# Kernel tuning notes

Measured on AMD Instinct MI355X. Metric: run time of the kernel, lower is better.

## Reference

```python
import jax, jax.numpy as jnp
import numpy as np

N, E, D = 50000, 800000, 128
H, C = 8, 16  # heads, hidden_per_head; H*C == D
NEG_SLOPE = 0.15


def setup_inputs() -> dict:
    key = jax.random.key(0)
    ks = jax.random.split(key, 8)
    x = jax.random.normal(ks[0], (N, D), dtype=jnp.float32)
    edge_index = jax.random.randint(ks[1], (2, E), 0, N, dtype=jnp.int32)
    s = 1.0 / np.sqrt(D)
    return {
        "x": x,
        "edge_index": edge_index,
        "ln_g": jnp.ones((D,), jnp.float32),
        "ln_b": jnp.zeros((D,), jnp.float32),
        "W_l": jax.random.normal(ks[2], (D, H * C), jnp.float32) * s,
        "b_l": jnp.zeros((H * C,), jnp.float32),
        "W_r": jax.random.normal(ks[3], (D, H * C), jnp.float32) * s,
        "b_r": jnp.zeros((H * C,), jnp.float32),
        "att": jax.random.normal(ks[4], (H, C), jnp.float32) * (1.0 / np.sqrt(C)),
        "bias": jnp.zeros((H * C,), jnp.float32),
    }


def _layernorm(x, g, b, eps=1e-5):
    mu = jnp.mean(x, axis=-1, keepdims=True)
    var = jnp.mean(jnp.square(x - mu), axis=-1, keepdims=True)
    return (x - mu) * jax.lax.rsqrt(var + eps) * g + b


def reference(x, edge_index, ln_g, ln_b, W_l, b_l, W_r, b_r, att, bias):
    src, dst = edge_index[0], edge_index[1]
    h = _layernorm(x, ln_g, ln_b)                      # [N, D]
    xl = (h @ W_l + b_l).reshape(N, H, C)              # source-side transform
    xr = (h @ W_r + b_r).reshape(N, H, C)              # target-side transform
    # GATv2 edge attention: leaky_relu(x_j + x_i) . att
    e = xl[src] + xr[dst]                              # [E, H, C]
    e_act = jnp.where(e > 0, e, NEG_SLOPE * e)
    alpha = jnp.einsum('ehc,hc->eh', e_act, att)       # [E, H]
    # segment softmax over edges grouped by destination node
    m = jax.ops.segment_max(alpha, dst, num_segments=N)   # [N, H]
    ex = jnp.exp(alpha - m[dst])                           # [E, H]
    denom = jax.ops.segment_sum(ex, dst, num_segments=N)  # [N, H]
    a = ex / (denom[dst] + 1e-16)                          # [E, H]
    # weighted message aggregation (scatter-add)
    msg = xl[src] * a[:, :, None]                          # [E, H, C]
    out = jax.ops.segment_sum(msg, dst, num_segments=N)   # [N, H, C]
    out = out.reshape(N, H * C) + bias
    h2 = jax.nn.relu(out)                                  # act='relu', dropout off (eval)
    return x + h2                                          # proj is Identity (in_dim == out_dim)
```

## Files before the change

### kernel.cpp

```cpp
#include <hip/hip_runtime.h>

typedef unsigned int uint32;
typedef __attribute__((ext_vector_type(4))) float f32x4;
typedef __attribute__((ext_vector_type(2))) float f32x2;
typedef __attribute__((ext_vector_type(8))) short bf16x8;
typedef __attribute__((ext_vector_type(4))) uint32 u32x4;

#define NEG_SLOPE 0.15f
#define GPB 2
#define SBUF_MAX 4096
#define CSR_MAX  6144

__device__ __forceinline__ float2 bf2_to_f2(uint32 u) {
  union { uint32 i; float f; } a, b;
  a.i = u << 16;
  b.i = u & 0xffff0000u;
  return make_float2(a.f, b.f);
}

__device__ __forceinline__ f32x2 unpk(uint32 u) {
  union { uint32 i; float f; } lo, hi;
  lo.i = u << 16; hi.i = u & 0xffff0000u;
  f32x2 r; r.x = lo.f; r.y = hi.f; return r;
}

__device__ __forceinline__ float bf_to_f(unsigned short s) {
  union { uint32 i; float f; } u;
  u.i = ((uint32)s) << 16;
  return u.f;
}

__device__ __forceinline__ unsigned short f32_to_bf16(float f) {
  union { float f; uint32 i; } u; u.f = f;
  uint32 r = u.i + 0x7fffu + ((u.i >> 16) & 1u);
  return (unsigned short)(r >> 16);
}

__device__ __forceinline__ uint32 pack_bf2(float x, float y) {
  return (uint32)f32_to_bf16(x) | ((uint32)f32_to_bf16(y) << 16);
}

__device__ __forceinline__ float2 loadpair(const void* p, size_t i, int isbf) {
  if (isbf) return bf2_to_f2(((const uint32*)p)[i]);
  return ((const float2*)p)[i];
}

__device__ __forceinline__ float2 loadpair_nt(const void* p, size_t i, int isbf) {
  if (isbf) {
    uint32 u = __builtin_nontemporal_load((const uint32*)p + i);
    return bf2_to_f2(u);
  }
  f32x2 v = __builtin_nontemporal_load((const f32x2*)p + i);
  return make_float2(v.x, v.y);
}

__device__ __forceinline__ float loadelem(const void* p, size_t i, int isbf) {
  if (isbf) return bf_to_f(((const unsigned short*)p)[i]);
  return ((const float*)p)[i];
}

__device__ __forceinline__ int get_isbf(const void* ln_g) {
  return ((const uint32*)ln_g)[0] != 0x3F800000u ? 1 : 0;
}

__device__ __forceinline__ float dpp_swap1(float x) {
  union { float f; int i; } u, r;
  u.f = x;
  r.i = __builtin_amdgcn_mov_dpp(u.i, 0xB1, 0xF, 0xF, false);
  return r.f;
}

__device__ __forceinline__ f32x2 pk_add(f32x2 a, f32x2 b) {
  f32x2 d;
  asm("v_pk_add_f32 %0, %1, %2" : "=v"(d) : "v"(a), "v"(b));
  return d;
}
__device__ __forceinline__ f32x2 pk_mul(f32x2 a, f32x2 b) {
  f32x2 d;
  asm("v_pk_mul_f32 %0, %1, %2" : "=v"(d) : "v"(a), "v"(b));
  return d;
}
__device__ __forceinline__ f32x2 pk_fma(f32x2 a, f32x2 b, f32x2 c) {
  f32x2 d;
  asm("v_pk_fma_f32 %0, %1, %2, %3" : "=v"(d) : "v"(a), "v"(b), "v"(c));
  return d;
}
__device__ __forceinline__ float exp2_raw(float x) {
  float r;
  asm("v_exp_f32 %0, %1" : "=v"(r) : "v"(x));
  return r;
}

__global__ __launch_bounds__(256) void prep_hist_k(
    const void* __restrict__ Wl, const void* __restrict__ Wr,
    const void* __restrict__ bl, const void* __restrict__ br,
    const void* __restrict__ att, const void* __restrict__ obias,
    const void* __restrict__ ln_g, const void* __restrict__ ln_b,
    unsigned short* __restrict__ Wt, float* __restrict__ c1,
    float* __restrict__ c2b, float* __restrict__ att_c,
    float* __restrict__ obias_c,
    const int* __restrict__ ei, int* __restrict__ cntg,
    int E, int Eb, int R)
{
  int b = blockIdx.x;
  if (b < 128) {
    int isbf = get_isbf(ln_g);
    int id = b * 256 + threadIdx.x;
    int n = id >> 7, k = id & 127;
    float g = loadelem(ln_g, k, isbf);
    float v = (n < 128) ? loadelem(Wl, (size_t)k * 128 + n, isbf)
                        : loadelem(Wr, (size_t)k * 128 + (n - 128), isbf);
    Wt[(size_t)n * 128 + k] = f32_to_bf16(g * v);
    if (id < 128) {
      att_c[id]   = loadelem(att, id, isbf) * 1.44269504088896f;
      obias_c[id] = loadelem(obias, id, isbf);
    }
  } else if (b < 192) {
    int isbf = get_isbf(ln_g);
    int w = threadIdx.x >> 6, lane = threadIdx.x & 63;
    int n = (b - 128) * 4 + w;
    const void* W = (n < 128) ? Wl : Wr;
    int nn = n & 127;
    float s1 = 0.f, s2 = 0.f;
    #pragma unroll
    for (int t = 0; t < 2; ++t) {
      int kk = t * 64 + lane;
      float wv = loadelem(W, (size_t)kk * 128 + nn, isbf);
      s1 += loadelem(ln_g, kk, isbf) * wv;
      s2 += loadelem(ln_b, kk, isbf) * wv;
    }
    #pragma unroll
    for (int off = 1; off < 64; off <<= 1) {
      s1 += __shfl_xor(s1, off, 64);
      s2 += __shfl_xor(s2, off, 64);
    }
    if (lane == 0) {
      c1[n] = s1;
      c2b[n] = s2 + ((n < 128) ? loadelem(bl, nn, isbf) : loadelem(br, nn, isbf));
    }
  } else {
    __shared__ int hist[256];
    int hb = b - 192, tid = threadIdx.x;
    hist[tid] = 0;
    __syncthreads();
    int startE = hb * Eb, endE = min(E, startE + Eb);
    const int* dp = ei + E;
    int nfull = (endE > startE) ? ((endE - startE) >> 2) : 0;
    for (int g = tid; g < nfull; g += 256) {
      int4 d = *(const int4*)(dp + startE + g * 4);
      atomicAdd(&hist[((uint32)d.x) >> 8], 1);
      atomicAdd(&hist[((uint32)d.y) >> 8], 1);
      atomicAdd(&hist[((uint32)d.z) >> 8], 1);
      atomicAdd(&hist[((uint32)d.w) >> 8], 1);
    }
    int rem0 = startE + nfull * 4;
    if (rem0 + tid < endE) atomicAdd(&hist[((uint32)dp[rem0 + tid]) >> 8], 1);
    __syncthreads();
    if (tid < R) cntg[tid * 256 + hb] = hist[tid];
  }
}

__global__ __launch_bounds__(1024) void scanA_k(const int* __restrict__ in,
    int* __restrict__ outl, int* __restrict__ psum, int n)
{
  __shared__ int wsum[16];
  int tid = threadIdx.x, lane = tid & 63, w = tid >> 6;
  int i = blockIdx.x * 1024 + tid;
  int v = (i < n) ? in[i] : 0;
  int xs = v;
  #pragma unroll
  for (int off = 1; off < 64; off <<= 1) {
    int y = __shfl_up(xs, off, 64);
    if (lane >= off) xs += y;
  }
  if (lane == 63) wsum[w] = xs;
  __syncthreads();
  if (w == 0) {
    int sv = (lane < 16) ? wsum[lane] : 0;
    int ss = sv;
    #pragma unroll
    for (int off = 1; off < 16; off <<= 1) {
      int y = __shfl_up(ss, off, 64);
      if (lane >= off) ss += y;
    }
    if (lane < 16) wsum[lane] = ss - sv;
    if (lane == 15) psum[blockIdx.x] = ss;
  }
  __syncthreads();
  if (i < n) outl[i] = wsum[w] + xs - v;
}

__device__ __forceinline__ void load_group(bf16x8* slot, const void* x,
                                           int isbf, int rl, int quad) {
  if (isbf) {
    const unsigned short* xp = (const unsigned short*)x + (size_t)rl * 128 + quad * 8;
    #pragma unroll
    for (int kc = 0; kc < 4; ++kc) slot[kc] = *(const bf16x8*)(xp + kc * 32);
  } else {
    const float* xp = (const float*)x + (size_t)rl * 128 + quad * 8;
    #pragma unroll
    for (int kc = 0; kc < 4; ++kc) {
      float4 a0 = *(const float4*)(xp + kc * 32);
      float4 a1 = *(const float4*)(xp + kc * 32 + 4);
      union { bf16x8 v; uint32 u[4]; } av;
      av.u[0] = pack_bf2(a0.x, a0.y);
      av.u[1] = pack_bf2(a0.z, a0.w);
      av.u[2] = pack_bf2(a1.x, a1.y);
      av.u[3] = pack_bf2(a1.z, a1.w);
      slot[kc] = av.v;
    }
  }
}

__global__ __launch_bounds__(256) void bin_gemm_k(
    const int* __restrict__ ei, const int* __restrict__ cntg,
    const int* __restrict__ cbase,
    const int* __restrict__ psum, uint32* __restrict__ binned,
    int E, int Eb, int R, int nbScan,
    const void* __restrict__ x, const void* __restrict__ ln_g,
    const unsigned short* __restrict__ Wt,
    const float* __restrict__ c1, const float* __restrict__ c2b,
    unsigned short* __restrict__ xl, unsigned short* __restrict__ xr,
    int nrows)
{
  if (blockIdx.x < 256) {
    __shared__ int spsum[64];
    __shared__ int wsum2[4];
    __shared__ int lofs[256];
    __shared__ int gbase[256];
    __shared__ int cur[256];
    __shared__ uint32 sbuf[SBUF_MAX];
    int b = blockIdx.x, tid = threadIdx.x;
    int lane = tid & 63, w = tid >> 6;

    if (tid < 64) {
      int v = (tid < nbScan) ? psum[tid] : 0;
      int xs = v;
      #pragma unroll
      for (int off = 1; off < 64; off <<= 1) {
        int y = __shfl_up(xs, off, 64);
        if (tid >= off) xs += y;
      }
      spsum[tid] = xs - v;
    }
    int v2 = (tid < R) ? cntg[tid * 256 + b] : 0;
    int xs2 = v2;
    #pragma unroll
    for (int off = 1; off < 64; off <<= 1) {
      int y = __shfl_up(xs2, off, 64);
      if (lane >= off) xs2 += y;
    }
    if (lane == 63) wsum2[w] = xs2;
    __syncthreads();

    int woff2 = 0;
    #pragma unroll
    for (int i = 0; i < 4; ++i) if (i < w) woff2 += wsum2[i];
    int lo = woff2 + xs2 - v2;
    lofs[tid] = lo;
    int startE = b * Eb, endE = min(E, startE + Eb);
    if (tid < R) {
      int idx = tid * 256 + b;
      gbase[tid] = cbase[idx] + spsum[idx >> 10];
    }

    if (Eb <= SBUF_MAX) {
      cur[tid] = lo;
      __syncthreads();
      for (int e = startE + tid; e < endE; e += 256) {
        uint32 src = (uint32)ei[e], dst = (uint32)ei[E + e];
        uint32 r = dst >> 8;
        int pos = atomicAdd(&cur[r], 1);
        sbuf[pos] = src | ((dst & 255u) << 16) | (r << 24);
      }
      __syncthreads();
      int nloc = endE - startE;
      for (int i = tid; i < nloc; i += 256) {
        uint32 e2 = sbuf[i];
        uint32 r = e2 >> 24;
        binned[gbase[r] + (i - lofs[r])] = e2 & 0x00FFFFFFu;
      }
    } else {
      cur[tid] = (tid < R) ? gbase[tid] : 0;
      __syncthreads();
      for (int e = startE + tid; e < endE; e += 256) {
        uint32 src = (uint32)ei[e], dst = (uint32)ei[E + e];
        int pos = atomicAdd(&cur[dst >> 8], 1);
        binned[pos] = src | ((dst & 255u) << 16);
      }
    }
    return;
  }

  __shared__ unsigned short ot[4][16][72];
  int bid  = blockIdx.x - 256;
  int isbf = get_isbf(ln_g);
  int lane = threadIdx.x & 63;
  int w    = threadIdx.x >> 6;
  int m16  = lane & 15;
  int quad = lane >> 4;
  int base = bid * (GPB * 16);

  bf16x8 araw[GPB][4];
  #pragma unroll
  for (int g2 = 0; g2 < GPB; ++g2) {
    int r = base + g2 * 16 + m16;
    if (r >= nrows) r = nrows - 1;
    load_group(araw[g2], x, isbf, r, quad);
  }

  bf16x8 bfrag[4][4];
  #pragma unroll
  for (int nt = 0; nt < 4; ++nt)
    #pragma unroll
    for (int kc = 0; kc < 4; ++kc)
      bfrag[nt][kc] = *(const bf16x8*)(
          Wt + (size_t)(w * 64 + nt * 16 + m16) * 128 + kc * 32 + quad * 8);

  float c1v[4], c2v[4];
  #pragma unroll
  for (int nt = 0; nt < 4; ++nt) {
    int col = w * 64 + nt * 16 + m16;
    c1v[nt] = c1[col];
    c2v[nt] = c2b[col];
  }

  unsigned short* dst = (w < 2) ? xl : xr;
  int cb = (w & 1) * 64;

  #pragma unroll
  for (int g2 = 0; g2 < GPB; ++g2) {
    bf16x8* A = araw[g2];

    float s = 0.f, s2 = 0.f;
    #pragma unroll
    for (int kc = 0; kc < 4; ++kc) {
      union { bf16x8 v; uint32 u[4]; } uu; uu.v = A[kc];
      #pragma unroll
      for (int j = 0; j < 4; ++j) {
        float2 t = bf2_to_f2(uu.u[j]);
        s += t.x + t.y;
        s2 += t.x * t.x + t.y * t.y;
      }
    }
    s  += __shfl_xor(s, 16, 64);  s2 += __shfl_xor(s2, 16, 64);
    s  += __shfl_xor(s, 32, 64);  s2 += __shfl_xor(s2, 32, 64);
    float mu  = s * (1.0f / 128.0f);
    float var = fmaxf(s2 * (1.0f / 128.0f) - mu * mu, 0.0f);
    float rs  = rsqrtf(var + 1e-5f);
    float rm  = rs * mu;

    f32x4 acc[4];
    #pragma unroll
    for (int nt = 0; nt < 4; ++nt) acc[nt] = (f32x4){0.f, 0.f, 0.f, 0.f};
    #pragma unroll
    for (int kc = 0; kc < 4; ++kc)
      #pragma unroll
      for (int nt = 0; nt < 4; ++nt)
        acc[nt] = __builtin_amdgcn_mfma_f32_16x16x32_bf16(A[kc], bfrag[nt][kc], acc[nt], 0, 0, 0);

    float rs_j[4], rm_j[4];
    #pragma unroll
    for (int j = 0; j < 4; ++j) {
      rs_j[j] = __shfl(rs, quad * 4 + j, 64);
      rm_j[j] = __shfl(rm, quad * 4 + j, 64);
    }

    #pragma unroll
    for (int nt = 0; nt < 4; ++nt) {
      #pragma unroll
      for (int j = 0; j < 4; ++j) {
        ot[w][quad * 4 + j][nt * 16 + m16] =
            f32_to_bf16(rs_j[j] * acc[nt][j] - rm_j[j] * c1v[nt] + c2v[nt]);
      }
    }
    #pragma unroll
    for (int h = 0; h < 2; ++h) {
      int row16 = h * 8 + (lane >> 3);
      int cp    = lane & 7;
      int r = base + g2 * 16 + row16;
      bf16x8 v = *(const bf16x8*)&ot[w][row16][cp * 8];
      if (r < nrows)
        *(bf16x8*)(dst + (size_t)r * 128 + cb + cp * 8) = v;
    }
  }
}

__global__ __launch_bounds__(1024) void rangesort_k(
    const uint32* __restrict__ binned, const int* __restrict__ cbase,
    const int* __restrict__ psum,
    int* __restrict__ starts, unsigned short* __restrict__ csr16,
    int E, int N, int R, int nbScan)
{
  __shared__ int hist[256];
  __shared__ int wsum[4];
  __shared__ int cur[256];
  __shared__ int spsum[64];
  __shared__ unsigned short csr_l[CSR_MAX];
  int r = blockIdx.x;
  int tid = threadIdx.x, lane = tid & 63, w = tid >> 6;

  if (tid < 64) {
    int pv = (tid < nbScan) ? psum[tid] : 0;
    int pxs = pv;
    #pragma unroll
    for (int off = 1; off < 64; off <<= 1) {
      int y = __shfl_up(pxs, off, 64);
      if (tid >= off) pxs += y;
    }
    spsum[tid] = pxs - pv;
  }
  if (tid < 256) hist[tid] = 0;
  __syncthreads();

  int i0 = r * 256;
  int segStart = cbase[i0] + spsum[i0 >> 10];
  int segEnd;
  if (r + 1 < R) {
    int i1 = (r + 1) * 256;
    segEnd = cbase[i1] + spsum[i1 >> 10];
  } else {
    segEnd = E;
  }
  int segLen = segEnd - segStart;
  bool lds_ok = (segLen <= CSR_MAX);
  if (r == 0) {
    if (tid == 0) starts[N] = E;
    if (tid < 32) csr16[E + tid] = 0;
  }

  for (int i = segStart + tid; i < segEnd; i += 1024)
    atomicAdd(&hist[(binned[i] >> 16) & 255u], 1);
  __syncthreads();

  int v = 0, xs = 0;
  if (tid < 256) {
    v = hist[tid];
    xs = v;
    #pragma unroll
    for (int off = 1; off < 64; off <<= 1) {
      int y = __shfl_up(xs, off, 64);
      if (lane >= off) xs += y;
    }
    if (lane == 63) wsum[w] = xs;
  }
  __syncthreads();
  if (tid < 256) {
    int woff = 0;
    #pragma unroll
    for (int i = 0; i < 4; ++i) if (i < w) woff += wsum[i];
    int st_local = woff + xs - v;
    int node = (r << 8) + tid;
    if (node < N) starts[node] = segStart + st_local;
    cur[tid] = lds_ok ? st_local : segStart + st_local;
  }
  __syncthreads();

  if (lds_ok) {
    for (int i = segStart + tid; i < segEnd; i += 1024) {
      uint32 pk = binned[i];
      int d = (pk >> 16) & 255u;
      int pos = atomicAdd(&cur[d], 1);
      csr_l[pos] = (unsigned short)(pk & 0xffffu);
    }
    __syncthreads();
    for (int i = tid; i < segLen; i += 1024)
      csr16[segStart + i] = csr_l[i];
  } else {
    for (int i = segStart + tid; i < segEnd; i += 1024) {
      uint32 pk = binned[i];
      int d = (pk >> 16) & 255u;
      int pos = atomicAdd(&cur[d], 1);
      csr16[pos] = (unsigned short)(pk & 0xffffu);
    }
  }
}

__global__ __launch_bounds__(256) void agg_k(
    const uint32* __restrict__ xl32,
    const uint32* __restrict__ xr32,
    const int* __restrict__ starts, const unsigned short* __restrict__ csr16,
    const void* __restrict__ x, const void* __restrict__ ln_g,
    const float* __restrict__ att_c, const float* __restrict__ obias_c,
    void* __restrict__ out, int n)
{
  int node = blockIdx.x * 4 + (threadIdx.x >> 6);
  if (node >= n) return;
  int isbf = get_isbf(ln_g);
  int lane = threadIdx.x & 63;
  int q    = lane >> 4;
  int sub  = lane & 15;

  u32x4 xru = __builtin_nontemporal_load(
      (const u32x4*)(xr32 + (size_t)node * 64 + sub * 4));
  f32x2 xr0 = unpk(xru.x), xr1 = unpk(xru.y), xr2 = unpk(xru.z), xr3 = unpk(xru.w);
  const f32x2* atp = (const f32x2*)(att_c + sub * 8);
  f32x2 t0 = atp[0], t1 = atp[1], t2 = atp[2], t3 = atp[3];
  f32x2 ns; ns.x = NEG_SLOPE; ns.y = NEG_SLOPE;

  float lsum = 0.f;
  f32x2 ac[4];
  #pragma unroll
  for (int i = 0; i < 4; ++i) { ac[i].x = 0.f; ac[i].y = 0.f; }

  int p0 = __builtin_amdgcn_readfirstlane(starts[node]);
  int p1 = __builtin_amdgcn_readfirstlane(starts[node + 1]);

#define AGG_BODY(XU, OK) do { \
    f32x2 a0 = unpk((XU).x), a1 = unpk((XU).y), a2 = unpk((XU).z), a3 = unpk((XU).w); \
    f32x2 e0 = pk_add(a0, xr0), e1 = pk_add(a1, xr1); \
    f32x2 e2 = pk_add(a2, xr2), e3 = pk_add(a3, xr3); \
    f32x2 m0 = pk_mul(e0, ns), m1 = pk_mul(e1, ns); \
    f32x2 m2 = pk_mul(e2, ns), m3 = pk_mul(e3, ns); \
    e0.x = fmaxf(e0.x, m0.x); e0.y = fmaxf(e0.y, m0.y); \
    e1.x = fmaxf(e1.x, m1.x); e1.y = fmaxf(e1.y, m1.y); \
    e2.x = fmaxf(e2.x, m2.x); e2.y = fmaxf(e2.y, m2.y); \
    e3.x = fmaxf(e3.x, m3.x); e3.y = fmaxf(e3.y, m3.y); \
    f32x2 dt = pk_mul(e0, t0); \
    dt = pk_fma(e1, t1, dt); \
    dt = pk_fma(e2, t2, dt); \
    dt = pk_fma(e3, t3, dt); \
    float dot = dt.x + dt.y; \
    dot += dpp_swap1(dot); \
    float pw = (OK) ? exp2_raw(dot) : 0.f; \
    lsum += pw; \
    f32x2 pw2; pw2.x = pw; pw2.y = pw; \
    ac[0] = pk_fma(pw2, a0, ac[0]); \
    ac[1] = pk_fma(pw2, a1, ac[1]); \
    ac[2] = pk_fma(pw2, a2, ac[2]); \
    ac[3] = pk_fma(pw2, a3, ac[3]); \
  } while (0)

  if (p0 < p1) {
    uint32 so = (uint32)(sub * 4);
    const unsigned short* csp = csr16 + p0 + q;
    uint32 j0 = csp[0];
    uint32 j1 = csp[4];
    uint32 j2 = csp[8];
    uint32 j3 = csp[12];
    uint4 xu0 = *(const uint4*)(xl32 + (size_t)(j0 * 64u + so));
    uint4 xu1 = *(const uint4*)(xl32 + (size_t)(j1 * 64u + so));
    int pq   = p0 + q;
    int p1m4 = p1 - 4;
    for (int p = p0; p < p1; p += 8) {
      uint4 xA = xu0;
      xu0 = *(const uint4*)(xl32 + (size_t)(j2 * 64u + so));
      j2  = csp[16];
      AGG_BODY(xA, pq < p1);
      uint4 xB = xu1;
      xu1 = *(const uint4*)(xl32 + (size_t)(j3 * 64u + so));
      j3  = csp[20];
      AGG_BODY(xB, pq < p1m4);
      csp += 8;
      pq  += 8;
    }
  }
#undef AGG_BODY

  lsum += __shfl_xor(lsum, 16, 64);
  lsum += __shfl_xor(lsum, 32, 64);
  #pragma unroll
  for (int i = 0; i < 4; ++i) {
    ac[i].x += __shfl_xor(ac[i].x, 16, 64);
    ac[i].x += __shfl_xor(ac[i].x, 32, 64);
    ac[i].y += __shfl_xor(ac[i].y, 16, 64);
    ac[i].y += __shfl_xor(ac[i].y, 32, 64);
  }

  if (q == 0) {
    float inv = 1.0f / (lsum + 1e-16f);
    float4 b0 = *(const float4*)(obias_c + sub * 8);
    float4 b1 = *(const float4*)(obias_c + sub * 8 + 4);
    float2 rx[4];
    #pragma unroll
    for (int i = 0; i < 4; ++i)
      rx[i] = loadpair_nt(x, (size_t)node * 64 + sub * 4 + i, isbf);
    float o0 = rx[0].x + fmaxf(ac[0].x * inv + b0.x, 0.f);
    float o1 = rx[0].y + fmaxf(ac[0].y * inv + b0.y, 0.f);
    float o2 = rx[1].x + fmaxf(ac[1].x * inv + b0.z, 0.f);
    float o3 = rx[1].y + fmaxf(ac[1].y * inv + b0.w, 0.f);
    float o4 = rx[2].x + fmaxf(ac[2].x * inv + b1.x, 0.f);
    float o5 = rx[2].y + fmaxf(ac[2].y * inv + b1.y, 0.f);
    float o6 = rx[3].x + fmaxf(ac[3].x * inv + b1.z, 0.f);
    float o7 = rx[3].y + fmaxf(ac[3].y * inv + b1.w, 0.f);
    if (isbf) {
      u32x4 ov;
      ov.x = pack_bf2(o0, o1); ov.y = pack_bf2(o2, o3);
      ov.z = pack_bf2(o4, o5); ov.w = pack_bf2(o6, o7);
      __builtin_nontemporal_store(ov, (u32x4*)((uint32*)out + (size_t)node * 64 + sub * 4));
    } else {
      f32x4 f0; f0.x = o0; f0.y = o1; f0.z = o2; f0.w = o3;
      f32x4 f1; f1.x = o4; f1.y = o5; f1.z = o6; f1.w = o7;
      __builtin_nontemporal_store(f0, (f32x4*)((float*)out + (size_t)node * 128 + sub * 8));
      __builtin_nontemporal_store(f1, (f32x4*)((float*)out + (size_t)node * 128 + sub * 8 + 4));
    }
  }
}

static inline char* align16(char* p) {
  return (char*)(((uintptr_t)p + 15) & ~(uintptr_t)15);
}

extern "C" void kernel_launch(void* const* d_in, const int* in_sizes, int n_in,
                              void* d_out, int out_size, void* d_ws, size_t ws_size,
                              hipStream_t stream) {
  const void* x    = d_in[0];
  const int*  ei   = (const int*)d_in[1];
  const void* ln_g = d_in[2];
  const void* ln_b = d_in[3];
  const void* Wl   = d_in[4];
  const void* bl   = d_in[5];
  const void* Wr   = d_in[6];
  const void* br   = d_in[7];
  const void* att  = d_in[8];
  const void* bias = d_in[9];

  int N = in_sizes[0] / 128;
  int E = in_sizes[1] / 2;
  int R = (N + 255) >> 8;
  int L = R * 256;
  int Eb = (((E + 255) / 256) + 3) & ~3;

  char* ws = (char*)d_ws;
  unsigned short* xl = (unsigned short*)ws; ws = align16(ws + (size_t)N * 128 * 2);
  unsigned short* xr = (unsigned short*)ws; ws = align16(ws + (size_t)N * 128 * 2);
  unsigned short* Wt = (unsigned short*)ws; ws = align16(ws + 256 * 128 * 2);
  float* c1      = (float*)ws;              ws = align16(ws + 256 * 4);
  float* c2b     = (float*)ws;              ws = align16(ws + 256 * 4);
  float* att_c   = (float*)ws;              ws = align16(ws + 128 * 4);
  float* obias_c = (float*)ws;              ws = align16(ws + 128 * 4);
  int* cntg      = (int*)ws;                ws = align16(ws + (size_t)L * 4);
  int* cbase     = (int*)ws;                ws = align16(ws + (size_t)L * 4);
  int* psum      = (int*)ws;                ws = align16(ws + 64 * 4);
  int* starts    = (int*)ws;                ws = align16(ws + (size_t)(N + 1) * 4);
  uint32* binned = (uint32*)ws;             ws = align16(ws + (size_t)E * 4);
  unsigned short* csr16 = (unsigned short*)ws; ws = align16(ws + (size_t)(E + 32) * 2);

  int nbScan = (L + 1023) / 1024;
  int nGemmB = (N + GPB * 16 - 1) / (GPB * 16);

  hipLaunchKernelGGL(prep_hist_k, dim3(448), dim3(256), 0, stream,
                     Wl, Wr, bl, br, att, bias, ln_g, ln_b,
                     Wt, c1, c2b, att_c, obias_c,
                     ei, cntg, E, Eb, R);
  hipLaunchKernelGGL(scanA_k, dim3(nbScan), dim3(1024), 0, stream, cntg, cbase, psum, L);
  hipLaunchKernelGGL(bin_gemm_k, dim3(256 + nGemmB), dim3(256), 0, stream,
                     ei, cntg, cbase, psum, binned, E, Eb, R, nbScan,
                     x, ln_g, Wt, c1, c2b, xl, xr, N);
  hipLaunchKernelGGL(rangesort_k, dim3(R), dim3(1024), 0, stream,
                     binned, cbase, psum, starts, csr16, E, N, R, nbScan);
  hipLaunchKernelGGL(agg_k, dim3((N + 3) / 4), dim3(256), 0, stream,
                     (const uint32*)xl, (const uint32*)xr, starts, csr16,
                     x, ln_g, att_c, obias_c, d_out, N);
}
```

Before: 170.5 us.

## Replace global scan kernel with per-range atomic totals and atomic slot reservation

Removes the scanA_k launch. The histogram blocks now atomically accumulate per-range totals, and each binning block scans those totals locally and reserves its slice within each range with an atomicAdd on a global cursor. The rangesort kernel derives its segment bounds from the same totals. This saves one kernel launch and the scan pass, but adds a memset and makes the order of edges within each range nondeterministic. That is harmless as long as rangesort fully re-sorts within each range.

After: 174.7 us. 1.02x slower.

```diff
diff --git a/kernel.cpp b/kernel.cpp
--- a/kernel.cpp
+++ b/kernel.cpp
@@ -100,6 +100,7 @@
     float* __restrict__ c2b, float* __restrict__ att_c,
     float* __restrict__ obias_c,
     const int* __restrict__ ei, int* __restrict__ cntg,
+    int* __restrict__ rtot,
     int E, int Eb, int R)
 {
   int b = blockIdx.x;
@@ -156,38 +157,12 @@
     int rem0 = startE + nfull * 4;
     if (rem0 + tid < endE) atomicAdd(&hist[((uint32)dp[rem0 + tid]) >> 8], 1);
     __syncthreads();
-    if (tid < R) cntg[tid * 256 + hb] = hist[tid];
-  }
-}
-
-__global__ __launch_bounds__(1024) void scanA_k(const int* __restrict__ in,
-    int* __restrict__ outl, int* __restrict__ psum, int n)
-{
-  __shared__ int wsum[16];
-  int tid = threadIdx.x, lane = tid & 63, w = tid >> 6;
-  int i = blockIdx.x * 1024 + tid;
-  int v = (i < n) ? in[i] : 0;
-  int xs = v;
-  #pragma unroll
-  for (int off = 1; off < 64; off <<= 1) {
-    int y = __shfl_up(xs, off, 64);
-    if (lane >= off) xs += y;
-  }
-  if (lane == 63) wsum[w] = xs;
-  __syncthreads();
-  if (w == 0) {
-    int sv = (lane < 16) ? wsum[lane] : 0;
-    int ss = sv;
-    #pragma unroll
-    for (int off = 1; off < 16; off <<= 1) {
-      int y = __shfl_up(ss, off, 64);
-      if (lane >= off) ss += y;
-    }
-    if (lane < 16) wsum[lane] = ss - sv;
-    if (lane == 15) psum[blockIdx.x] = ss;
-  }
-  __syncthreads();
-  if (i < n) outl[i] = wsum[w] + xs - v;
+    if (tid < R) {
+      int h = hist[tid];
+      cntg[tid * 256 + hb] = h;
+      if (h) atomicAdd(&rtot[tid], h);
+    }
+  }
 }
 
 __device__ __forceinline__ void load_group(bf16x8* slot, const void* x,
@@ -214,9 +189,9 @@
 
 __global__ __launch_bounds__(256) void bin_gemm_k(
     const int* __restrict__ ei, const int* __restrict__ cntg,
-    const int* __restrict__ cbase,
-    const int* __restrict__ psum, uint32* __restrict__ binned,
-    int E, int Eb, int R, int nbScan,
+    const int* __restrict__ rtot, int* __restrict__ gcur,
+    uint32* __restrict__ binned,
+    int E, int Eb, int R,
     const void* __restrict__ x, const void* __restrict__ ln_g,
     const unsigned short* __restrict__ Wt,
     const float* __restrict__ c1, const float* __restrict__ c2b,
@@ -224,8 +199,9 @@
     int nrows)
 {
   if (blockIdx.x < 256) {
-    __shared__ int spsum[64];
-    __shared__ int wsum2[4];
+    __shared__ int wsumA[4];
+    __shared__ int wsumB[4];
+    __shared__ int rb[256];
     __shared__ int lofs[256];
     __shared__ int gbase[256];
     __shared__ int cur[256];
@@ -233,16 +209,14 @@
     int b = blockIdx.x, tid = threadIdx.x;
     int lane = tid & 63, w = tid >> 6;
 
-    if (tid < 64) {
-      int v = (tid < nbScan) ? psum[tid] : 0;
-      int xs = v;
-      #pragma unroll
-      for (int off = 1; off < 64; off <<= 1) {
-        int y = __shfl_up(xs, off, 64);
-        if (tid >= off) xs += y;
-      }
-      spsum[tid] = xs - v;
-    }
+    int rt = (tid < R) ? rtot[tid] : 0;
+    int xs1 = rt;
+    #pragma unroll
+    for (int off = 1; off < 64; off <<= 1) {
+      int y = __shfl_up(xs1, off, 64);
+      if (lane >= off) xs1 += y;
+    }
+    if (lane == 63) wsumA[w] = xs1;
     int v2 = (tid < R) ? cntg[tid * 256 + b] : 0;
     int xs2 = v2;
     #pragma unroll
@@ -250,19 +224,21 @@
       int y = __shfl_up(xs2, off, 64);
       if (lane >= off) xs2 += y;
     }
-    if (lane == 63) wsum2[w] = xs2;
+    if (lane == 63) wsumB[w] = xs2;
     __syncthreads();
 
-    int woff2 = 0;
-    #pragma unroll
-    for (int i = 0; i < 4; ++i) if (i < w) woff2 += wsum2[i];
-    int lo = woff2 + xs2 - v2;
+    int woffA = 0, woffB = 0;
+    #pragma unroll
+    for (int i = 0; i < 4; ++i) {
+      if (i < w) { woffA += wsumA[i]; woffB += wsumB[i]; }
+    }
+    rb[tid] = woffA + xs1 - rt;
+    int lo = woffB + xs2 - v2;
     lofs[tid] = lo;
+    int res = 0;
+    if (tid < R && v2 > 0) res = atomicAdd(&gcur[tid], v2);
+    gbase[tid] = rb[tid] + res;
     int startE = b * Eb, endE = min(E, startE + Eb);
-    if (tid < R) {
-      int idx = tid * 256 + b;
-      gbase[tid] = cbase[idx] + spsum[idx >> 10];
-    }
 
     if (Eb <= SBUF_MAX) {
       cur[tid] = lo;
@@ -281,7 +257,7 @@
         binned[gbase[r] + (i - lofs[r])] = e2 & 0x00FFFFFFu;
       }
     } else {
-      cur[tid] = (tid < R) ? gbase[tid] : 0;
+      cur[tid] = gbase[tid];
       __syncthreads();
       for (int e = startE + tid; e < endE; e += 256) {
         uint32 src = (uint32)ei[e], dst = (uint32)ei[E + e];
@@ -387,41 +363,41 @@
 }
 
 __global__ __launch_bounds__(1024) void rangesort_k(
-    const uint32* __restrict__ binned, const int* __restrict__ cbase,
-    const int* __restrict__ psum,
+    const uint32* __restrict__ binned, const int* __restrict__ rtot,
     int* __restrict__ starts, unsigned short* __restrict__ csr16,
-    int E, int N, int R, int nbScan)
+    int E, int N, int R)
 {
   __shared__ int hist[256];
   __shared__ int wsum[4];
+  __shared__ int wsumR[4];
   __shared__ int cur[256];
-  __shared__ int spsum[64];
+  __shared__ int segb[2];
   __shared__ unsigned short csr_l[CSR_MAX];
   int r = blockIdx.x;
   int tid = threadIdx.x, lane = tid & 63, w = tid >> 6;
 
-  if (tid < 64) {
-    int pv = (tid < nbScan) ? psum[tid] : 0;
-    int pxs = pv;
+  int rt = 0, xsr = 0;
+  if (tid < 256) {
+    rt = (tid < R) ? rtot[tid] : 0;
+    xsr = rt;
     #pragma unroll
     for (int off = 1; off < 64; off <<= 1) {
-      int y = __shfl_up(pxs, off, 64);
-      if (tid >= off) pxs += y;
-    }
-    spsum[tid] = pxs - pv;
-  }
-  if (tid < 256) hist[tid] = 0;
+      int y = __shfl_up(xsr, off, 64);
+      if (lane >= off) xsr += y;
+    }
+    if (lane == 63) wsumR[w] = xsr;
+    hist[tid] = 0;
+  }
   __syncthreads();
-
-  int i0 = r * 256;
-  int segStart = cbase[i0] + spsum[i0 >> 10];
-  int segEnd;
-  if (r + 1 < R) {
-    int i1 = (r + 1) * 256;
-    segEnd = cbase[i1] + spsum[i1 >> 10];
-  } else {
-    segEnd = E;
-  }
+  if (tid < 256) {
+    int woff = 0;
+    #pragma unroll
+    for (int i = 0; i < 4; ++i) if (i < w) woff += wsumR[i];
+    int ex = woff + xsr - rt;
+    if (tid == r) { segb[0] = ex; segb[1] = ex + rt; }
+  }
+  __syncthreads();
+  int segStart = segb[0], segEnd = segb[1];
   int segLen = segEnd - segStart;
   bool lds_ok = (segLen <= CSR_MAX);
   if (r == 0) {
@@ -630,25 +606,24 @@
   float* att_c   = (float*)ws;              ws = align16(ws + 128 * 4);
   float* obias_c = (float*)ws;              ws = align16(ws + 128 * 4);
   int* cntg      = (int*)ws;                ws = align16(ws + (size_t)L * 4);
-  int* cbase     = (int*)ws;                ws = align16(ws + (size_t)L * 4);
-  int* psum      = (int*)ws;                ws = align16(ws + 64 * 4);
+  int* rtot      = (int*)ws;                ws = align16(ws + 512 * 4);
+  int* gcur      = rtot + 256;
   int* starts    = (int*)ws;                ws = align16(ws + (size_t)(N + 1) * 4);
   uint32* binned = (uint32*)ws;             ws = align16(ws + (size_t)E * 4);
   unsigned short* csr16 = (unsigned short*)ws; ws = align16(ws + (size_t)(E + 32) * 2);
 
-  int nbScan = (L + 1023) / 1024;
   int nGemmB = (N + GPB * 16 - 1) / (GPB * 16);
 
+  hipMemsetAsync(rtot, 0, 512 * 4, stream);
   hipLaunchKernelGGL(prep_hist_k, dim3(448), dim3(256), 0, stream,
                      Wl, Wr, bl, br, att, bias, ln_g, ln_b,
                      Wt, c1, c2b, att_c, obias_c,
-                     ei, cntg, E, Eb, R);
-  hipLaunchKernelGGL(scanA_k, dim3(nbScan), dim3(1024), 0, stream, cntg, cbase, psum, L);
+                     ei, cntg, rtot, E, Eb, R);
   hipLaunchKernelGGL(bin_gemm_k, dim3(256 + nGemmB), dim3(256), 0, stream,
-                     ei, cntg, cbase, psum, binned, E, Eb, R, nbScan,
+                     ei, cntg, rtot, gcur, binned, E, Eb, R,
                      x, ln_g, Wt, c1, c2b, xl, xr, N);
   hipLaunchKernelGGL(rangesort_k, dim3(R), dim3(1024), 0, stream,
-                     binned, cbase, psum, starts, csr16, E, N, R, nbScan);
+                     binned, rtot, starts, csr16, E, N, R);
   hipLaunchKernelGGL(agg_k, dim3((N + 3) / 4), dim3(256), 0, stream,
                      (const uint32*)xl, (const uint32*)xr, starts, csr16,
                      x, ln_g, att_c, obias_c, d_out, N);
```
